# Optimization experiments

Hardware: AMD Instinct MI355X
Metric: run time of the kernel (lower is better)

The kernel has to match this reference:

```python
import jax, jax.numpy as jnp
import numpy as np

N, E, C, NNZ, D = 100000, 50000, 2000, 1600000, 128


def _seg_mean(vals, idx, num):
    s = jax.ops.segment_sum(vals, idx, num_segments=num)
    cnt = jax.ops.segment_sum(jnp.ones((vals.shape[0],), vals.dtype), idx, num_segments=num)
    return s / jnp.maximum(cnt, 1.0)[:, None]


def _prelu(x, a):
    return jnp.where(x >= 0, x, a * x)


def setup_inputs() -> dict:
    key = jax.random.key(0)
    ks = jax.random.split(key, 32)
    x = jax.random.normal(ks[0], (N, D), jnp.float32)
    src = jax.random.randint(ks[1], (NNZ,), 0, N)
    dst = jax.random.randint(ks[2], (NNZ,), 0, E)
    hyperedge_index = jnp.stack([src, dst])
    hyperedge_component_index = jnp.stack([jnp.arange(E), jax.random.randint(ks[3], (E,), 0, C)])
    node_component_index = jnp.stack([jnp.arange(N), jax.random.randint(ks[4], (N,), 0, C)])
    inp = {
        'x': x,
        'hyperedge_index': hyperedge_index,
        'hyperedge_component_index': hyperedge_component_index,
        'node_component_index': node_component_index,
        'num_nodes': N, 'num_edges': E, 'num_components': C,
        'prelu_a': jnp.float32(0.25),
    }
    ki = 5
    for layer in range(2):
        for name in ['v2e', 'e2v', 'e2c', 'n2c']:
            inp[f'W_{name}_{layer}'] = jax.random.normal(ks[ki], (D, D), jnp.float32) / np.sqrt(D).astype(np.float32)
            inp[f'b_{name}_{layer}'] = jnp.zeros((D,), jnp.float32)
            ki += 1
    return inp


def reference(x, hyperedge_index, hyperedge_component_index, node_component_index,
              num_nodes, num_edges, num_components, prelu_a,
              W_v2e_0, b_v2e_0, W_e2v_0, b_e2v_0, W_e2c_0, b_e2c_0, W_n2c_0, b_n2c_0,
              W_v2e_1, b_v2e_1, W_e2v_1, b_e2v_1, W_e2c_1, b_e2c_1, W_n2c_1, b_n2c_1):
    Nn, Ne, Nc = num_nodes, num_edges, num_components
    # self-loop construction: node i joins fresh hyperedge Ne + i
    src = jnp.concatenate([hyperedge_index[0], jnp.arange(Nn)])
    dst = jnp.concatenate([hyperedge_index[1], jnp.arange(Ne, Ne + Nn)])
    E_tot = Ne + Nn
    he_e, he_c = hyperedge_component_index[0], hyperedge_component_index[1]
    nc_n, nc_c = node_component_index[0], node_component_index[1]

    def conv(h, Wv, bv, We, be, Wec, bec, Wnc, bnc):
        # node -> edge: transform, gather along incidences, scatter-mean to edges
        e = _prelu(_seg_mean((h @ Wv + bv)[src], dst, E_tot), prelu_a)
        # edge -> node
        n = _seg_mean((e @ We + be)[dst], src, Nn)
        # edge -> component  +  node -> component
        c = _prelu(_seg_mean((e @ Wec + bec)[he_e], he_c, Nc)
                   + _seg_mean((n @ Wnc + bnc)[nc_n], nc_c, Nc), prelu_a)
        return n, e, c

    n, e, c = conv(x, W_v2e_0, b_v2e_0, W_e2v_0, b_e2v_0, W_e2c_0, b_e2c_0, W_n2c_0, b_n2c_0)
    h = _prelu(n, prelu_a)
    n, e, c = conv(h, W_v2e_1, b_v2e_1, W_e2v_1, b_e2v_1, W_e2c_1, b_e2c_1, W_n2c_1, b_n2c_1)
    return _prelu(n, prelu_a), e[:Ne], c
```

## Files before the change

### kernel.cpp

```cpp
#include <hip/hip_runtime.h>
#include <hip/hip_bf16.h>

#define NN 100000
#define EE 50000
#define CC 2000
#define NNZ 1600000
#define DD 128
#define ET (EE + NN)

#define PB 800
#define CHUNK 2000
#define NBK 196
#define SCAP 12288

__device__ __forceinline__ float prelu(float x, float a) {
    return x >= 0.f ? x : a * x;
}

__device__ __forceinline__ float bf2f(unsigned short h) {
    return __uint_as_float(((unsigned int)h) << 16);
}
__device__ __forceinline__ unsigned short f2bf(float f) {
    unsigned int u = __float_as_uint(f);
    u = (u + 0x7fff + ((u >> 16) & 1)) >> 16;
    return (unsigned short)u;
}

struct alignas(16) us8 { ushort4 lo, hi; };

__global__ __launch_bounds__(256) void part_hist(const int* __restrict__ src,
                                                 const int* __restrict__ dst,
                                                 int* __restrict__ etot,
                                                 int* __restrict__ ntot,
                                                 const int* __restrict__ hec,
                                                 const int* __restrict__ ncc,
                                                 int* __restrict__ c1cnt,
                                                 int* __restrict__ c2cnt) {
    __shared__ int he[NBK], hn[NBK];
    for (int i = threadIdx.x; i < NBK; i += 256) { he[i] = 0; hn[i] = 0; }
    __syncthreads();
    int b = blockIdx.x;
    int beg = b * CHUNK, end = min(beg + CHUNK, NNZ);
    for (int k = beg + threadIdx.x; k < end; k += 256) {
        atomicAdd(&he[dst[k] >> 8], 1);
        atomicAdd(&hn[src[k] >> 9], 1);
    }
    int gid = b * 256 + threadIdx.x;
    int gstride = PB * 256;
    for (int k = gid; k < EE; k += gstride) atomicAdd(&c1cnt[hec[k]], 1);
    for (int k = gid; k < NN; k += gstride) atomicAdd(&c2cnt[ncc[k]], 1);
    __syncthreads();
    for (int i = threadIdx.x; i < NBK; i += 256) {
        if (he[i]) atomicAdd(&etot[i], he[i]);
        if (hn[i]) atomicAdd(&ntot[i], hn[i]);
    }
}

__global__ __launch_bounds__(256) void scan_small(const int* __restrict__ etot,
        const int* __restrict__ ntot, int* __restrict__ ebase, int* __restrict__ nbase,
        int* __restrict__ ecur, int* __restrict__ ncur) {
    __shared__ int se[256], sn[256];
    int t = threadIdx.x;
    int ve = (t < NBK) ? etot[t] : 0;
    int vn = (t < NBK) ? ntot[t] : 0;
    se[t] = ve; sn[t] = vn;
    __syncthreads();
    for (int off = 1; off < 256; off <<= 1) {
        int ae = (t >= off) ? se[t - off] : 0;
        int an = (t >= off) ? sn[t - off] : 0;
        __syncthreads();
        se[t] += ae; sn[t] += an;
        __syncthreads();
    }
    if (t < NBK) {
        int be = se[t] - ve, bn = sn[t] - vn;
        ebase[t] = be; ecur[t] = be;
        nbase[t] = bn; ncur[t] = bn;
    }
    if (t == 0) { ebase[NBK] = NNZ; nbase[NBK] = NNZ; }
}

__global__ __launch_bounds__(256) void reorder_kernel(const int* __restrict__ src,
        const int* __restrict__ dst, int* __restrict__ ecur, int* __restrict__ ncur,
        int2* __restrict__ pe, int2* __restrict__ pn) {
    __shared__ int sS[CHUNK], sD[CHUNK];
    __shared__ int he[NBK], hn[NBK];
    __shared__ int beA[NBK], bnA[NBK];
    int b = blockIdx.x;
    int beg = b * CHUNK;
    int n = min(CHUNK, NNZ - beg);
    for (int i = threadIdx.x; i < NBK; i += 256) { he[i] = 0; hn[i] = 0; }
    for (int i = threadIdx.x; i < n; i += 256) {
        sS[i] = src[beg + i];
        sD[i] = dst[beg + i];
    }
    __syncthreads();
    for (int i = threadIdx.x; i < n; i += 256) {
        atomicAdd(&he[sD[i] >> 8], 1);
        atomicAdd(&hn[sS[i] >> 9], 1);
    }
    __syncthreads();
    for (int i = threadIdx.x; i < NBK; i += 256) {
        beA[i] = he[i] ? atomicAdd(&ecur[i], he[i]) : 0;
        bnA[i] = hn[i] ? atomicAdd(&ncur[i], hn[i]) : 0;
        he[i] = 0; hn[i] = 0;
    }
    __syncthreads();
    for (int i = threadIdx.x; i < n; i += 256) {
        int d = sD[i], s = sS[i];
        int bk = d >> 8;
        int p = beA[bk] + atomicAdd(&he[bk], 1);
        pe[p] = make_int2(d, s);
        bk = s >> 9;
        p = bnA[bk] + atomicAdd(&hn[bk], 1);
        pn[p] = make_int2(s, d);
    }
}

template <int W, int SHIFT>
__global__ __launch_bounds__(256) void bucket_scatter(const int2* __restrict__ pairs,
        const int* __restrict__ bases, int* __restrict__ ptr_excl,
        int* __restrict__ csr, int segn) {
    __shared__ int cnt[W];
    __shared__ int stage[SCAP];
    int b = blockIdx.x;
    int base = bases[b];
    int bend = bases[b + 1];
    int bsize = bend - base;

    for (int i = threadIdx.x; i < W; i += 256) cnt[i] = 0;
    __syncthreads();
    for (int k = base + threadIdx.x; k < bend; k += 256)
        atomicAdd(&cnt[pairs[k].x - (b << SHIFT)], 1);
    __syncthreads();

    int l0 = threadIdx.x, l1 = threadIdx.x + 256;
    int o0 = cnt[l0];
    int o1 = (W > 256) ? cnt[l1] : 0;
    for (int off = 1; off < W; off <<= 1) {
        int v0 = (l0 >= off) ? cnt[l0 - off] : 0;
        int v1 = 0;
        if (W > 256 && l1 >= off) v1 = cnt[l1 - off];
        __syncthreads();
        cnt[l0] += v0;
        if (W > 256) cnt[l1] += v1;
        __syncthreads();
    }
    int e0 = cnt[l0] - o0;
    int e1 = (W > 256) ? (cnt[l1] - o1) : 0;
    __syncthreads();
    cnt[l0] = base + e0;
    if (W > 256) cnt[l1] = base + e1;
    int g0 = (b << SHIFT) + l0;
    if (g0 < segn) ptr_excl[g0] = base + e0;
    if (W > 256) {
        int g1 = (b << SHIFT) + l1;
        if (g1 < segn) ptr_excl[g1] = base + e1;
    }
    if (b == NBK - 1 && threadIdx.x == 0) ptr_excl[segn] = NNZ;
    __syncthreads();

    bool fb = (bsize > SCAP);
    for (int k = base + threadIdx.x; k < bend; k += 256) {
        int2 pr = pairs[k];
        int pos = atomicAdd(&cnt[pr.x - (b << SHIFT)], 1);
        if (!fb) stage[pos - base] = pr.y;
        else     csr[pos] = pr.y;
    }
    __syncthreads();
    if (!fb)
        for (int t = threadIdx.x; t < bsize; t += 256) csr[base + t] = stage[t];
}

template <bool PRELU_IN, bool PRELU_OUT, bool OUT_BF16>
__global__ __launch_bounds__(256) void gemm128(
        const float* __restrict__ H, const float* __restrict__ W,
        const float* __restrict__ bias, void* __restrict__ outv,
        float* __restrict__ out2 ,
        const int* __restrict__ gate ,
        int M, const float* __restrict__ a_ptr) {
    __shared__ float Wl[128 * 128];
    for (int i = threadIdx.x; i < 4096; i += 256)
        ((float4*)Wl)[i] = ((const float4*)W)[i];
    float a = 0.f;
    if (PRELU_IN || PRELU_OUT) a = *a_ptr;
    __syncthreads();

    const int jc = threadIdx.x & 15;
    const int rg = threadIdx.x >> 4;
    const int j0 = jc * 8;
    const int row0 = blockIdx.x * 64 + rg * 4;

    float acc[4][8];
#pragma unroll
    for (int r = 0; r < 4; ++r)
#pragma unroll
        for (int c = 0; c < 8; ++c) acc[r][c] = 0.f;

    int rclamp[4];
#pragma unroll
    for (int r = 0; r < 4; ++r) {
        int row = row0 + r;
        rclamp[r] = row < M ? row : (M - 1);
    }

#pragma unroll 2
    for (int k0 = 0; k0 < 128; k0 += 4) {
        float hr[4][4];
#pragma unroll
        for (int r = 0; r < 4; ++r) {
            float4 v = *(const float4*)(H + (size_t)rclamp[r] * DD + k0);
            if (PRELU_IN) {
                v.x = prelu(v.x, a); v.y = prelu(v.y, a);
                v.z = prelu(v.z, a); v.w = prelu(v.w, a);
            }
            hr[r][0] = v.x; hr[r][1] = v.y; hr[r][2] = v.z; hr[r][3] = v.w;
        }
#pragma unroll
        for (int kk = 0; kk < 4; ++kk) {
            const float4 w0 = *(const float4*)&Wl[(k0 + kk) * 128 + j0];
            const float4 w1 = *(const float4*)&Wl[(k0 + kk) * 128 + j0 + 4];
#pragma unroll
            for (int r = 0; r < 4; ++r) {
                float h = hr[r][kk];
                acc[r][0] += h * w0.x; acc[r][1] += h * w0.y;
                acc[r][2] += h * w0.z; acc[r][3] += h * w0.w;
                acc[r][4] += h * w1.x; acc[r][5] += h * w1.y;
                acc[r][6] += h * w1.z; acc[r][7] += h * w1.w;
            }
        }
    }

    float bb[8];
#pragma unroll
    for (int c = 0; c < 8; ++c) bb[c] = bias[j0 + c];

#pragma unroll
    for (int r = 0; r < 4; ++r) {
        int row = row0 + r;
        if (row < M) {
            float g = 1.f;
            if (gate) g = (gate[row] > 0) ? 1.f : 0.f;
            float o[8];
#pragma unroll
            for (int c = 0; c < 8; ++c) o[c] = acc[r][c] + bb[c] * g;
            if (OUT_BF16) {
                us8 o8;
                o8.lo = make_ushort4(f2bf(o[0]), f2bf(o[1]), f2bf(o[2]), f2bf(o[3]));
                o8.hi = make_ushort4(f2bf(o[4]), f2bf(o[5]), f2bf(o[6]), f2bf(o[7]));
                *(us8*)((unsigned short*)outv + (size_t)row * DD + j0) = o8;
            } else {
                float* out = (float*)outv;
                *(float4*)(out + (size_t)row * DD + j0)     = make_float4(o[0], o[1], o[2], o[3]);
                *(float4*)(out + (size_t)row * DD + j0 + 4) = make_float4(o[4], o[5], o[6], o[7]);
            }
            if (PRELU_OUT) {
                *(float4*)(out2 + (size_t)row * DD + j0) =
                    make_float4(prelu(o[0], a), prelu(o[1], a), prelu(o[2], a), prelu(o[3], a));
                *(float4*)(out2 + (size_t)row * DD + j0 + 4) =
                    make_float4(prelu(o[4], a), prelu(o[5], a), prelu(o[6], a), prelu(o[7], a));
            }
        }
    }
}

__global__ __launch_bounds__(256) void edge_agg(const unsigned short* __restrict__ hv,
        const int* __restrict__ eptr, const int* __restrict__ ecsr,
        unsigned short* __restrict__ Eb, float* __restrict__ out_e,
        const float* __restrict__ a_ptr) {
    int j = blockIdx.x * 4 + (threadIdx.x >> 6);
    int lane = threadIdx.x & 63;
    int g = lane >> 4, l16 = lane & 15;
    int p0 = eptr[j], p1 = eptr[j + 1];
    float a = *a_ptr;
    float s0=0.f,s1=0.f,s2=0.f,s3=0.f,s4=0.f,s5=0.f,s6=0.f,s7=0.f;
    for (int p = p0 + g; p < p1; p += 4) {
        int row = ecsr[p];
        const us8 v = *(const us8*)(hv + (size_t)row * DD + l16 * 8);
        s0 += bf2f(v.lo.x); s1 += bf2f(v.lo.y);
        s2 += bf2f(v.lo.z); s3 += bf2f(v.lo.w);
        s4 += bf2f(v.hi.x); s5 += bf2f(v.hi.y);
        s6 += bf2f(v.hi.z); s7 += bf2f(v.hi.w);
    }
#pragma unroll
    for (int off = 16; off < 64; off <<= 1) {
        s0 += __shfl_xor(s0, off); s1 += __shfl_xor(s1, off);
        s2 += __shfl_xor(s2, off); s3 += __shfl_xor(s3, off);
        s4 += __shfl_xor(s4, off); s5 += __shfl_xor(s5, off);
        s6 += __shfl_xor(s6, off); s7 += __shfl_xor(s7, off);
    }
    if (g == 0) {
        float inv = 1.0f / fmaxf((float)(p1 - p0), 1.0f);
        float o[8] = { prelu(s0*inv,a), prelu(s1*inv,a), prelu(s2*inv,a), prelu(s3*inv,a),
                       prelu(s4*inv,a), prelu(s5*inv,a), prelu(s6*inv,a), prelu(s7*inv,a) };
        us8 ob;
        ob.lo = make_ushort4(f2bf(o[0]), f2bf(o[1]), f2bf(o[2]), f2bf(o[3]));
        ob.hi = make_ushort4(f2bf(o[4]), f2bf(o[5]), f2bf(o[6]), f2bf(o[7]));
        *(us8*)(Eb + (size_t)j * DD + l16 * 8) = ob;
        if (out_e) {
            float* w = out_e + (size_t)j * DD + l16 * 8;
            *(float4*)(w)     = make_float4(o[0], o[1], o[2], o[3]);
            *(float4*)(w + 4) = make_float4(o[4], o[5], o[6], o[7]);
        }
    }
}

__global__ __launch_bounds__(256) void node_agg(const unsigned short* __restrict__ Eb,
        const unsigned short* __restrict__ hv, const int* __restrict__ nptr,
        const int* __restrict__ ncsr, float* __restrict__ nagg,
        const float* __restrict__ a_ptr) {
    int i = blockIdx.x * 4 + (threadIdx.x >> 6);
    int lane = threadIdx.x & 63;
    int g = lane >> 4, l16 = lane & 15;
    int p0 = nptr[i], p1 = nptr[i + 1];
    float a = *a_ptr;
    float s0=0.f,s1=0.f,s2=0.f,s3=0.f,s4=0.f,s5=0.f,s6=0.f,s7=0.f;
    if (g == 0) {
        const us8 v = *(const us8*)(hv + (size_t)i * DD + l16 * 8);
        s0 = prelu(bf2f(v.lo.x), a); s1 = prelu(bf2f(v.lo.y), a);
        s2 = prelu(bf2f(v.lo.z), a); s3 = prelu(bf2f(v.lo.w), a);
        s4 = prelu(bf2f(v.hi.x), a); s5 = prelu(bf2f(v.hi.y), a);
        s6 = prelu(bf2f(v.hi.z), a); s7 = prelu(bf2f(v.hi.w), a);
    }
    for (int p = p0 + g; p < p1; p += 4) {
        int row = ncsr[p];
        const us8 v = *(const us8*)(Eb + (size_t)row * DD + l16 * 8);
        s0 += bf2f(v.lo.x); s1 += bf2f(v.lo.y);
        s2 += bf2f(v.lo.z); s3 += bf2f(v.lo.w);
        s4 += bf2f(v.hi.x); s5 += bf2f(v.hi.y);
        s6 += bf2f(v.hi.z); s7 += bf2f(v.hi.w);
    }
#pragma unroll
    for (int off = 16; off < 64; off <<= 1) {
        s0 += __shfl_xor(s0, off); s1 += __shfl_xor(s1, off);
        s2 += __shfl_xor(s2, off); s3 += __shfl_xor(s3, off);
        s4 += __shfl_xor(s4, off); s5 += __shfl_xor(s5, off);
        s6 += __shfl_xor(s6, off); s7 += __shfl_xor(s7, off);
    }
    if (g == 0) {
        float inv = 1.0f / (float)(p1 - p0 + 1);
        float* w = nagg + (size_t)i * DD + l16 * 8;
        *(float4*)(w)     = make_float4(s0 * inv, s1 * inv, s2 * inv, s3 * inv);
        *(float4*)(w + 4) = make_float4(s4 * inv, s5 * inv, s6 * inv, s7 * inv);
    }
}

__global__ void comp_scatter(const float* __restrict__ rows, const int* __restrict__ comp,
                             float* __restrict__ acc, int M) {
    int i = blockIdx.x * blockDim.x + threadIdx.x;
    int stride = gridDim.x * blockDim.x;
    int total = M * DD;
    for (int k = i; k < total; k += stride) {
        int r = k >> 7, d = k & 127;
        atomicAdd(&acc[(size_t)comp[r] * DD + d], rows[k]);
    }
}

__global__ void comp_scatter_bf16(const unsigned short* __restrict__ rows,
                                  const int* __restrict__ comp,
                                  float* __restrict__ acc, int M) {
    int i = blockIdx.x * blockDim.x + threadIdx.x;
    int stride = gridDim.x * blockDim.x;
    int total = M * DD;
    for (int k = i; k < total; k += stride) {
        int r = k >> 7, d = k & 127;
        atomicAdd(&acc[(size_t)comp[r] * DD + d], bf2f(rows[k]));
    }
}

__global__ void cmean(float* __restrict__ c1, float* __restrict__ c2,
                      const int* __restrict__ cnt1, const int* __restrict__ cnt2) {
    int k = blockIdx.x * blockDim.x + threadIdx.x;
    if (k >= CC * DD) return;
    int r = k >> 7;
    c1[k] *= 1.0f / (float)max(cnt1[r], 1);
    c2[k] *= 1.0f / (float)max(cnt2[r], 1);
}

__global__ void c_final(const float* __restrict__ c1, const float* __restrict__ c2,
                        float* __restrict__ out, const float* __restrict__ a_ptr) {
    float a = *a_ptr;
    int k = blockIdx.x * blockDim.x + threadIdx.x;
    if (k >= CC * DD) return;
    out[k] = prelu(c1[k] + c2[k], a);
}

extern "C" void kernel_launch(void* const* d_in, const int* in_sizes, int n_in,
                              void* d_out, int out_size, void* d_ws, size_t ws_size,
                              hipStream_t stream) {
    const float* x     = (const float*)d_in[0];
    const int* he_idx  = (const int*)d_in[1];
    const int* hcomp   = (const int*)d_in[2];
    const int* ncomp   = (const int*)d_in[3];
    const float* a_ptr = (const float*)d_in[7];

    const float *W[8], *B[8];
    for (int l = 0; l < 2; ++l)
        for (int m = 0; m < 4; ++m) {
            W[l * 4 + m] = (const float*)d_in[8 + l * 8 + m * 2];
            B[l * 4 + m] = (const float*)d_in[8 + l * 8 + m * 2 + 1];
        }

    const int* src = he_idx;
    const int* dst = he_idx + NNZ;
    const int* hec = hcomp + EE;
    const int* ncc = ncomp + NN;

    unsigned short* Hb = (unsigned short*)d_ws;
    unsigned short* Eb = Hb + (size_t)NN * DD;
    float* Ag = (float*)(Eb + (size_t)EE * DD);
    float* Nb = Ag + (size_t)NN * DD;
    float* zreg = Nb + (size_t)NN * DD;
    float* c1acc = zreg;
    float* c2acc = c1acc + CC * DD;
    int* c1cnt   = (int*)(c2acc + CC * DD);
    int* c2cnt   = c1cnt + CC;
    int* etot    = c2cnt + CC;
    int* ntot    = etot + NBK;
    size_t zbytes = (size_t)(2 * CC * DD + 2 * CC + 2 * NBK) * 4;
    int* ebase   = ntot + NBK;
    int* nbase   = ebase + (NBK + 1);
    int* ecur    = nbase + (NBK + 1);
    int* ncur    = ecur + NBK;
    float* c1row = (float*)(ncur + NBK);
    float* c2row = c1row + CC * DD;
    int* eptr    = (int*)(c2row + CC * DD);
    int* nptr    = eptr + (EE + 1);
    int* csr_e   = nptr + (NN + 1);
    int* csr_n   = csr_e + NNZ;

    int2* pairs_e = (int2*)Ag;
    int2* pairs_n = pairs_e + NNZ;

    float* out_n = (float*)d_out;
    float* out_e = out_n + (size_t)NN * DD;
    float* out_c = out_e + (size_t)EE * DD;

    hipMemsetAsync(zreg, 0, zbytes, stream);
    part_hist<<<PB, 256, 0, stream>>>(src, dst, etot, ntot, hec, ncc, c1cnt, c2cnt);
    scan_small<<<1, 256, 0, stream>>>(etot, ntot, ebase, nbase, ecur, ncur);
    reorder_kernel<<<PB, 256, 0, stream>>>(src, dst, ecur, ncur, pairs_e, pairs_n);
    bucket_scatter<256, 8><<<NBK, 256, 0, stream>>>(pairs_e, ebase, eptr, csr_e, EE);
    bucket_scatter<512, 9><<<NBK, 256, 0, stream>>>(pairs_n, nbase, nptr, csr_n, NN);

    const int gN  = (NN + 63) / 64;
    const int gC  = (CC + 63) / 64;
    const int gEA = EE / 4;
    const int gNA = NN / 4;

    gemm128<false, false, true><<<gN, 256, 0, stream>>>(x, W[0], B[0], Hb, nullptr, nullptr, NN, a_ptr);
    edge_agg<<<gEA, 256, 0, stream>>>(Hb, eptr, csr_e, Eb, nullptr, a_ptr);
    node_agg<<<gNA, 256, 0, stream>>>(Eb, Hb, nptr, csr_n, Ag, a_ptr);
    gemm128<false, false, false><<<gN, 256, 0, stream>>>(Ag, W[1], B[1], Nb, nullptr, nullptr, NN, a_ptr);

    gemm128<true, false, true><<<gN, 256, 0, stream>>>(Nb, W[4], B[4], Hb, nullptr, nullptr, NN, a_ptr);
    edge_agg<<<gEA, 256, 0, stream>>>(Hb, eptr, csr_e, Eb, out_e, a_ptr);
    node_agg<<<gNA, 256, 0, stream>>>(Eb, Hb, nptr, csr_n, Ag, a_ptr);
    gemm128<false, true, false><<<gN, 256, 0, stream>>>(Ag, W[5], B[5], Nb, out_n, nullptr, NN, a_ptr);

    comp_scatter_bf16<<<2048, 256, 0, stream>>>(Eb, hec, c1acc, EE);
    comp_scatter<<<2048, 256, 0, stream>>>(Nb, ncc, c2acc, NN);
    cmean<<<(CC * DD + 255) / 256, 256, 0, stream>>>(c1acc, c2acc, c1cnt, c2cnt);
    gemm128<false, false, false><<<gC, 256, 0, stream>>>(c1acc, W[6], B[6], c1row, nullptr, c1cnt, CC, a_ptr);
    gemm128<false, false, false><<<gC, 256, 0, stream>>>(c2acc, W[7], B[7], c2row, nullptr, c2cnt, CC, a_ptr);
    c_final<<<(CC * DD + 255) / 256, 256, 0, stream>>>(c1row, c2row, out_c, a_ptr);
}
```

Before: 897.0 us.

## Replace FP32 node GEMMs with split-bf16 MFMA matrix-core kernel

Adds a gemm_mfma kernel that splits the fp32 inputs and weights into bf16 hi/lo parts and runs three MFMA 16x16x32 bf16 products per tile, which approximates fp32 accuracy. It is used for the four large 100000x128x128 node GEMMs, while the small component GEMMs keep the scalar FMA kernel. The aim is to move these GEMMs off the vector ALUs and onto the matrix cores. In exchange, each block builds a transposed, padded bf16 copy of W in shared memory, and the epilogue uses scalar strided stores instead of vectorized ones.

```diff
diff --git a/kernel.cpp b/kernel.cpp
--- a/kernel.cpp
+++ b/kernel.cpp
@@ -12,6 +12,11 @@
 #define CHUNK 2000
 #define NBK 196
 #define SCAP 12288
+
+#define WSTR 136
+
+typedef __attribute__((ext_vector_type(8))) __bf16 bf16x8;
+typedef __attribute__((ext_vector_type(4))) float f32x4;
 
 __device__ __forceinline__ float prelu(float x, float a) {
     return x >= 0.f ? x : a * x;
@@ -172,18 +177,98 @@
         for (int t = threadIdx.x; t < bsize; t += 256) csr[base + t] = stage[t];
 }
 
-template <bool PRELU_IN, bool PRELU_OUT, bool OUT_BF16>
+template <bool PRELU_IN, int OUTMODE>
+__global__ __launch_bounds__(256) void gemm_mfma(
+        const float* __restrict__ H, const float* __restrict__ W,
+        const float* __restrict__ bias, void* __restrict__ outv,
+        float* __restrict__ out2, int M, const float* __restrict__ a_ptr) {
+    __shared__ __bf16 Whi[128 * WSTR];
+    __shared__ __bf16 Wlo[128 * WSTR];
+    float a = 0.f;
+    if (PRELU_IN || OUTMODE == 2) a = *a_ptr;
+
+    for (int idx = threadIdx.x; idx < 4096; idx += 256) {
+        float4 v = ((const float4*)W)[idx];
+        int k = idx >> 5, n0 = (idx & 31) << 2;
+        float vv[4] = {v.x, v.y, v.z, v.w};
+#pragma unroll
+        for (int i = 0; i < 4; ++i) {
+            int n = n0 + i;
+            __bf16 h = (__bf16)vv[i];
+            __bf16 l = (__bf16)(vv[i] - (float)h);
+            Whi[n * WSTR + k] = h;
+            Wlo[n * WSTR + k] = l;
+        }
+    }
+    __syncthreads();
+
+    const int wave = threadIdx.x >> 6;
+    const int lane = threadIdx.x & 63;
+    const int lm = lane & 15, lq = lane >> 4;
+    const int m0 = blockIdx.x * 64 + wave * 16;
+    int mr = m0 + lm;
+    if (mr >= M) mr = M - 1;
+
+    f32x4 acc[8];
+#pragma unroll
+    for (int t = 0; t < 8; ++t) acc[t] = (f32x4)(0.f);
+
+#pragma unroll
+    for (int ks = 0; ks < 4; ++ks) {
+        const int k0 = ks * 32;
+        const float4 h0 = *(const float4*)(H + (size_t)mr * DD + k0 + lq * 8);
+        const float4 h1 = *(const float4*)(H + (size_t)mr * DD + k0 + lq * 8 + 4);
+        float hv[8] = {h0.x, h0.y, h0.z, h0.w, h1.x, h1.y, h1.z, h1.w};
+        bf16x8 ahi, alo;
+#pragma unroll
+        for (int i = 0; i < 8; ++i) {
+            float x = hv[i];
+            if (PRELU_IN) x = prelu(x, a);
+            __bf16 h = (__bf16)x;
+            ahi[i] = h;
+            alo[i] = (__bf16)(x - (float)h);
+        }
+#pragma unroll
+        for (int t = 0; t < 8; ++t) {
+            const int n = t * 16 + lm;
+            const int pos = n * WSTR + k0 + lq * 8;
+            const bf16x8 bhi = *(const bf16x8*)&Whi[pos];
+            const bf16x8 blo = *(const bf16x8*)&Wlo[pos];
+            acc[t] = __builtin_amdgcn_mfma_f32_16x16x32_bf16(ahi, bhi, acc[t], 0, 0, 0);
+            acc[t] = __builtin_amdgcn_mfma_f32_16x16x32_bf16(alo, bhi, acc[t], 0, 0, 0);
+            acc[t] = __builtin_amdgcn_mfma_f32_16x16x32_bf16(ahi, blo, acc[t], 0, 0, 0);
+        }
+    }
+
+#pragma unroll
+    for (int t = 0; t < 8; ++t) {
+        const int n = t * 16 + lm;
+        const float bn = bias[n];
+#pragma unroll
+        for (int r = 0; r < 4; ++r) {
+            const int m = m0 + lq * 4 + r;
+            if (m < M) {
+                float o = acc[t][r] + bn;
+                if (OUTMODE == 1) {
+                    ((__bf16*)outv)[(size_t)m * DD + n] = (__bf16)o;
+                } else {
+                    ((float*)outv)[(size_t)m * DD + n] = o;
+                    if (OUTMODE == 2)
+                        out2[(size_t)m * DD + n] = prelu(o, a);
+                }
+            }
+        }
+    }
+}
+
 __global__ __launch_bounds__(256) void gemm128(
         const float* __restrict__ H, const float* __restrict__ W,
-        const float* __restrict__ bias, void* __restrict__ outv,
-        float* __restrict__ out2 ,
+        const float* __restrict__ bias, float* __restrict__ out,
         const int* __restrict__ gate ,
-        int M, const float* __restrict__ a_ptr) {
+        int M) {
     __shared__ float Wl[128 * 128];
     for (int i = threadIdx.x; i < 4096; i += 256)
         ((float4*)Wl)[i] = ((const float4*)W)[i];
-    float a = 0.f;
-    if (PRELU_IN || PRELU_OUT) a = *a_ptr;
     __syncthreads();
 
     const int jc = threadIdx.x & 15;
@@ -210,10 +295,6 @@
 #pragma unroll
         for (int r = 0; r < 4; ++r) {
             float4 v = *(const float4*)(H + (size_t)rclamp[r] * DD + k0);
-            if (PRELU_IN) {
-                v.x = prelu(v.x, a); v.y = prelu(v.y, a);
-                v.z = prelu(v.z, a); v.w = prelu(v.w, a);
-            }
             hr[r][0] = v.x; hr[r][1] = v.y; hr[r][2] = v.z; hr[r][3] = v.w;
         }
 #pragma unroll
@@ -244,22 +325,8 @@
             float o[8];
 #pragma unroll
             for (int c = 0; c < 8; ++c) o[c] = acc[r][c] + bb[c] * g;
-            if (OUT_BF16) {
-                us8 o8;
-                o8.lo = make_ushort4(f2bf(o[0]), f2bf(o[1]), f2bf(o[2]), f2bf(o[3]));
-                o8.hi = make_ushort4(f2bf(o[4]), f2bf(o[5]), f2bf(o[6]), f2bf(o[7]));
-                *(us8*)((unsigned short*)outv + (size_t)row * DD + j0) = o8;
-            } else {
-                float* out = (float*)outv;
-                *(float4*)(out + (size_t)row * DD + j0)     = make_float4(o[0], o[1], o[2], o[3]);
-                *(float4*)(out + (size_t)row * DD + j0 + 4) = make_float4(o[4], o[5], o[6], o[7]);
-            }
-            if (PRELU_OUT) {
-                *(float4*)(out2 + (size_t)row * DD + j0) =
-                    make_float4(prelu(o[0], a), prelu(o[1], a), prelu(o[2], a), prelu(o[3], a));
-                *(float4*)(out2 + (size_t)row * DD + j0 + 4) =
-                    make_float4(prelu(o[4], a), prelu(o[5], a), prelu(o[6], a), prelu(o[7], a));
-            }
+            *(float4*)(out + (size_t)row * DD + j0)     = make_float4(o[0], o[1], o[2], o[3]);
+            *(float4*)(out + (size_t)row * DD + j0 + 4) = make_float4(o[4], o[5], o[6], o[7]);
         }
     }
 }
@@ -448,20 +515,20 @@
     const int gEA = EE / 4;
     const int gNA = NN / 4;
 
-    gemm128<false, false, true><<<gN, 256, 0, stream>>>(x, W[0], B[0], Hb, nullptr, nullptr, NN, a_ptr);
+    gemm_mfma<false, 1><<<gN, 256, 0, stream>>>(x, W[0], B[0], Hb, nullptr, NN, a_ptr);
     edge_agg<<<gEA, 256, 0, stream>>>(Hb, eptr, csr_e, Eb, nullptr, a_ptr);
     node_agg<<<gNA, 256, 0, stream>>>(Eb, Hb, nptr, csr_n, Ag, a_ptr);
-    gemm128<false, false, false><<<gN, 256, 0, stream>>>(Ag, W[1], B[1], Nb, nullptr, nullptr, NN, a_ptr);
-
-    gemm128<true, false, true><<<gN, 256, 0, stream>>>(Nb, W[4], B[4], Hb, nullptr, nullptr, NN, a_ptr);
+    gemm_mfma<false, 0><<<gN, 256, 0, stream>>>(Ag, W[1], B[1], Nb, nullptr, NN, a_ptr);
+
+    gemm_mfma<true, 1><<<gN, 256, 0, stream>>>(Nb, W[4], B[4], Hb, nullptr, NN, a_ptr);
     edge_agg<<<gEA, 256, 0, stream>>>(Hb, eptr, csr_e, Eb, out_e, a_ptr);
     node_agg<<<gNA, 256, 0, stream>>>(Eb, Hb, nptr, csr_n, Ag, a_ptr);
-    gemm128<false, true, false><<<gN, 256, 0, stream>>>(Ag, W[5], B[5], Nb, out_n, nullptr, NN, a_ptr);
+    gemm_mfma<false, 2><<<gN, 256, 0, stream>>>(Ag, W[5], B[5], Nb, out_n, NN, a_ptr);
 
     comp_scatter_bf16<<<2048, 256, 0, stream>>>(Eb, hec, c1acc, EE);
     comp_scatter<<<2048, 256, 0, stream>>>(Nb, ncc, c2acc, NN);
     cmean<<<(CC * DD + 255) / 256, 256, 0, stream>>>(c1acc, c2acc, c1cnt, c2cnt);
-    gemm128<false, false, false><<<gC, 256, 0, stream>>>(c1acc, W[6], B[6], c1row, nullptr, c1cnt, CC, a_ptr);
-    gemm128<false, false, false><<<gC, 256, 0, stream>>>(c2acc, W[7], B[7], c2row, nullptr, c2cnt, CC, a_ptr);
+    gemm128<<<gC, 256, 0, stream>>>(c1acc, W[6], B[6], c1row, c1cnt, CC);
+    gemm128<<<gC, 256, 0, stream>>>(c2acc, W[7], B[7], c2row, c2cnt, CC);
     c_final<<<(CC * DD + 255) / 256, 256, 0, stream>>>(c1row, c2row, out_c, a_ptr);
 }
```

Result: slower. 922.9 us (+2.9%).
